# Optimization experiments

Hardware: AMD Instinct MI355X
Metric: run time of the kernel (lower is better)

The kernel has to match this reference:

```python
import jax, jax.numpy as jnp
import numpy as np

N_NODES = 100000
EPS = 1e-12


def gcn_conv(x, src, dst, ew, W, b, n):
    """PyG GCNConv with edge weights: add self-loops (w=1), symmetric norm,
    scatter-add messages from src to dst, then bias."""
    loop = jnp.arange(n)
    src2 = jnp.concatenate([src, loop])
    dst2 = jnp.concatenate([dst, loop])
    ew2 = jnp.concatenate([ew, jnp.ones((n,), dtype=ew.dtype)])
    deg = jax.ops.segment_sum(ew2, dst2, num_segments=n)
    dinv = jnp.where(deg > 0, jax.lax.rsqrt(jnp.where(deg > 0, deg, 1.0)), 0.0)
    norm = dinv[src2] * ew2 * dinv[dst2]  # [E+N]
    xw = x @ W.T                           # [N, H]
    msg = xw[src2] * norm[:, None]         # [E+N, H]  (memory-bound gather)
    out = jax.ops.segment_sum(msg, dst2, num_segments=n)
    return out + b


def setup_inputs() -> dict:
    key = jax.random.key(0)
    ks = jax.random.split(key, 12)
    N, E, D_IN, H, FE = N_NODES, 1600000, 256, 128, 8
    x = jax.random.normal(ks[0], (N, D_IN), dtype=jnp.float32)
    edge_index = jax.random.randint(ks[1], (2, E), 0, N, dtype=jnp.int64)
    edge_attr = jax.random.uniform(ks[2], (E, FE), dtype=jnp.float32)
    s_in = 1.0 / np.sqrt(D_IN)
    s_h = 1.0 / np.sqrt(H)
    W_in = jax.random.uniform(ks[3], (H, D_IN), minval=-s_in, maxval=s_in)
    b_in = jax.random.uniform(ks[4], (H,), minval=-s_in, maxval=s_in)
    W1 = jax.random.uniform(ks[5], (H, H), minval=-s_h, maxval=s_h)
    b1 = jax.random.uniform(ks[6], (H,), minval=-s_h, maxval=s_h)
    W2 = jax.random.uniform(ks[7], (H, H), minval=-s_h, maxval=s_h)
    b2 = jax.random.uniform(ks[8], (H,), minval=-s_h, maxval=s_h)
    W_out = jax.random.uniform(ks[9], (H, H), minval=-s_h, maxval=s_h)
    b_out = jax.random.uniform(ks[10], (H,), minval=-s_h, maxval=s_h)
    return {"x": x, "edge_index": edge_index, "edge_attr": edge_attr,
            "W_in": W_in, "b_in": b_in, "W1": W1, "b1": b1,
            "W2": W2, "b2": b2, "W_out": W_out, "b_out": b_out}


def reference(x, edge_index, edge_attr, W_in, b_in, W1, b1, W2, b2, W_out, b_out):
    n = x.shape[0]
    src, dst = edge_index[0], edge_index[1]
    # edge weights: sum over edge features, then L2-normalize over edges
    ew = edge_attr.sum(axis=1)
    ew = ew / jnp.maximum(jnp.linalg.norm(ew), EPS)
    h = jax.nn.relu(x @ W_in.T + b_in)      # dropout = identity (eval)
    h = jax.nn.relu(gcn_conv(h, src, dst, ew, W1, b1, n))
    h = gcn_conv(h, src, dst, ew, W2, b2, n)
    return h @ W_out.T + b_out
```

## Files before the change

### kernel.cpp

```cpp
#include <hip/hip_runtime.h>
#include <hip/hip_bf16.h>
#include <math.h>


#define CAP 64
#define BN 256
#define BCAP 5120
#define CHUNK 2048
#define SRC_MASK 0x1FFFFu
#define Q_SCALE 16777216.0f
#define Q_INV   5.9604644775390625e-8f
#define GSTRIDE 1024

typedef __attribute__((ext_vector_type(8))) short bf16x8;
typedef __attribute__((ext_vector_type(2))) float f32x2;
typedef __attribute__((ext_vector_type(4))) float f32x4;
typedef __attribute__((ext_vector_type(4))) unsigned int u32x4;

#if __has_builtin(__builtin_amdgcn_cvt_pk_f32_fp8)
#define DEC_SCALE 5.9604644775390625e-8f
__device__ __forceinline__ f32x2 dec2(unsigned short t) {
  return __builtin_amdgcn_cvt_pk_f32_fp8((int)(unsigned)t, false);
}
#else
#define DEC_SCALE 7.922816251426434e28f
__device__ __forceinline__ f32x2 dec2(unsigned short t) {
  f32x2 r;
  r.x = __builtin_bit_cast(float, (((unsigned)t & 0x80u) << 24) | (((unsigned)t & 0x7Fu) << 20));
  r.y = __builtin_bit_cast(float, (((unsigned)t & 0x8000u) << 16) | (((unsigned)t & 0x7F00u) << 12));
  return r;
}
#endif

__device__ __forceinline__ unsigned rne_bf16(float f) {
  const unsigned u = __builtin_bit_cast(unsigned, f);
  return (u + 0x7FFFu + ((u >> 16) & 1u)) >> 16;
}
__device__ __forceinline__ unsigned packsplit(float f) {
  const unsigned hb = rne_bf16(f);
  const float hf = __builtin_bit_cast(float, hb << 16);
  const unsigned lb = rne_bf16(f - hf);
  return (hb << 16) | (lb & 0xFFFFu);
}
__device__ __forceinline__ float unpk(unsigned p) {
  return __builtin_bit_cast(float, p & 0xFFFF0000u) +
         __builtin_bit_cast(float, p << 16);
}
__device__ __forceinline__ void split8(const f32x4 a, const f32x4 b,
                                       bf16x8& hi, bf16x8& lo) {
#pragma unroll
  for (int i = 0; i < 8; ++i) {
    const float f = (i < 4) ? a[i] : b[i - 4];
    const unsigned hb = rne_bf16(f);
    hi[i] = (short)hb;
    const float hf = __builtin_bit_cast(float, hb << 16);
    lo[i] = (short)rne_bf16(f - hf);
  }
}
__device__ __forceinline__ unsigned char enc_e4m3(float v) {
  const float a = v * 0x1p-120f;
  unsigned bits = __builtin_bit_cast(unsigned, a);
  const unsigned sgn = (bits >> 24) & 0x80u;
  bits &= 0x7FFFFFFFu;
  unsigned u7 = (bits + 0x7FFFFu + ((bits >> 20) & 1u)) >> 20;
  if (u7 > 0x7Eu) u7 = 0x7Eu;
  return (unsigned char)(sgn | u7);
}

__global__ void ew_wsplit_kernel(const float* __restrict__ ea, float* __restrict__ ew,
                                 float* __restrict__ partial, int E,
                                 const float* __restrict__ W_in, const float* __restrict__ W1,
                                 const float* __restrict__ W2, const float* __restrict__ W_out,
                                 short* __restrict__ whi, short* __restrict__ wlo) {
  __shared__ float red[256];
  const int tid = threadIdx.x;
  if (blockIdx.x < 1024) {
    float ss = 0.f;
    const int stride = 1024 * 256;
    for (int e = blockIdx.x * 256 + tid; e < E; e += stride) {
      const float4 a = *(const float4*)(ea + (size_t)e * 8);
      const float4 b = *(const float4*)(ea + (size_t)e * 8 + 4);
      const float s = ((a.x + a.y) + (a.z + a.w)) + ((b.x + b.y) + (b.z + b.w));
      ew[e] = s;
      ss = fmaf(s, s, ss);
    }
    red[tid] = ss;
    __syncthreads();
    for (int k = 128; k > 0; k >>= 1) {
      if (tid < k) red[tid] += red[tid + k];
      __syncthreads();
    }
    if (tid == 0) partial[blockIdx.x] = red[0];
  } else {
    const int i = (blockIdx.x - 1024) * 256 + tid;
    if (i < 81920) {
      float f;
      if (i < 32768) f = W_in[i];
      else if (i < 49152) f = W1[i - 32768];
      else if (i < 65536) f = W2[i - 49152];
      else f = W_out[i - 65536];
      const unsigned hb = rne_bf16(f);
      whi[i] = (short)hb;
      wlo[i] = (short)rne_bf16(f - __builtin_bit_cast(float, hb << 16));
    }
  }
}

__global__ void norm_cursor_kernel(const float* __restrict__ partial,
                                   float* __restrict__ invnorm,
                                   unsigned* __restrict__ cursors, int NB) {
  __shared__ float red[256];
  const int tid = threadIdx.x;
  if (blockIdx.x == 0) {
    float s = partial[tid] + partial[tid + 256] + partial[tid + 512] + partial[tid + 768];
    red[tid] = s;
    __syncthreads();
    for (int k = 128; k > 0; k >>= 1) {
      if (tid < k) red[tid] += red[tid + k];
      __syncthreads();
    }
    if (tid == 0) invnorm[0] = 1.0f / fmaxf(sqrtf(red[0]), 1e-12f);
  } else {
    const int i = (blockIdx.x - 1) * 256 + tid;
    if (i < NB) cursors[i * 16] = (unsigned)i * BCAP;
  }
}

__global__ __launch_bounds__(512, 4) void bin_gemmin_kernel(
    const int* __restrict__ src, const int* __restrict__ dst,
    const float* __restrict__ ew, const float* __restrict__ invnorm,
    unsigned* __restrict__ cursors, unsigned long long* __restrict__ buckets,
    int E, int NB, int nbin,
    const float* __restrict__ X, const short* __restrict__ Whi,
    const short* __restrict__ Wlo, const float* __restrict__ bias,
    unsigned* __restrict__ Ypk, int ntiles) {
  __shared__ __align__(16) char smem[36864];
  const int tid = threadIdx.x;
  if ((int)blockIdx.x < nbin) {
    unsigned long long* recs = (unsigned long long*)smem;
    unsigned* hist = (unsigned*)(smem + 32768);
    unsigned* base = (unsigned*)(smem + 34816);
    const int e0 = blockIdx.x * CHUNK;
    const int n = min(CHUNK, E - e0);
    for (int i = tid; i < NB; i += 512) hist[i] = 0;
    __syncthreads();
    const float inv = invnorm[0];
    for (int i = tid; i < n; i += 512) {
      const int s = src[e0 + i];
      const int d = dst[e0 + i];
      const float w = ew[e0 + i] * inv;
      const unsigned q = (unsigned)fminf(fmaf(w, Q_SCALE, 0.5f), 32767.0f);
      recs[i] = ((unsigned long long)(((unsigned)d << 15) | q) << 32) | (unsigned)s;
      atomicAdd(&hist[d >> 8], 1u);
    }
    __syncthreads();
    for (int i = tid; i < NB; i += 512) {
      const unsigned c = hist[i];
      base[i] = c ? atomicAdd(&cursors[i * 16], c) : 0u;
      hist[i] = 0;
    }
    __syncthreads();
    for (int i = tid; i < n; i += 512) {
      const unsigned long long r = recs[i];
      const unsigned b = ((unsigned)(r >> 32) >> 15) >> 8;
      const unsigned pos = base[b] + atomicAdd(&hist[b], 1u);
      if (pos < (b + 1) * BCAP) buckets[pos] = r;
    }
  } else {
    constexpr int K = 256, KT = 8, RT = 2, CPR = 32;
    short* hi_p = (short*)smem;
    short* lo_p = (short*)(smem + 16384);
    const int lane = tid & 63, wave = tid >> 6;
    const int lrow = lane & 15, loct = lane >> 4;

    bf16x8 bhi[KT], blo[KT];
    const int col = wave * 16 + lrow;
#pragma unroll
    for (int kt = 0; kt < KT; ++kt) {
      const int off = col * K + kt * 32 + loct * 8;
      bhi[kt] = *(const bf16x8*)&Whi[off];
      blo[kt] = *(const bf16x8*)&Wlo[off];
    }
    const float bv = bias[col];

    const int r0c = tid >> 5, r1c = (tid + 512) >> 5;
    const int cc = tid & 31;
    f32x4 sa[2][2];
    const int vb = (int)blockIdx.x - nbin;

    int t = vb;
    {
      const int tl = (t < ntiles) ? t : 0;
      const float* xp0 = X + ((size_t)tl * 32 + r0c) * K + cc * 8;
      const float* xp1 = X + ((size_t)tl * 32 + r1c) * K + cc * 8;
      sa[0][0] = *(const f32x4*)xp0; sa[0][1] = *(const f32x4*)(xp0 + 4);
      sa[1][0] = *(const f32x4*)xp1; sa[1][1] = *(const f32x4*)(xp1 + 4);
    }
    while (t < ntiles) {
      {
        const int slot0 = r0c * CPR + (cc ^ (r0c & 7));
        const int slot1 = r1c * CPR + (cc ^ (r1c & 7));
        bf16x8 h, l;
        split8(sa[0][0], sa[0][1], h, l);
        *(bf16x8*)&hi_p[slot0 * 8] = h;
        *(bf16x8*)&lo_p[slot0 * 8] = l;
        split8(sa[1][0], sa[1][1], h, l);
        *(bf16x8*)&hi_p[slot1 * 8] = h;
        *(bf16x8*)&lo_p[slot1 * 8] = l;
      }
      __syncthreads();
      const int tn = t + GSTRIDE;
      {
        const int tl = (tn < ntiles) ? tn : 0;
        const float* xp0 = X + ((size_t)tl * 32 + r0c) * K + cc * 8;
        const float* xp1 = X + ((size_t)tl * 32 + r1c) * K + cc * 8;
        sa[0][0] = *(const f32x4*)xp0; sa[0][1] = *(const f32x4*)(xp0 + 4);
        sa[1][0] = *(const f32x4*)xp1; sa[1][1] = *(const f32x4*)(xp1 + 4);
      }
      f32x4 acc[RT];
#pragma unroll
      for (int rt = 0; rt < RT; ++rt) acc[rt] = f32x4{0.f, 0.f, 0.f, 0.f};
#pragma unroll
      for (int kt = 0; kt < KT; ++kt) {
        bf16x8 ahi[RT], alo[RT];
#pragma unroll
        for (int rt = 0; rt < RT; ++rt) {
          const int lr = rt * 16 + lrow;
          const int off = (lr * CPR + ((kt * 4 + loct) ^ (lr & 7))) * 8;
          ahi[rt] = *(const bf16x8*)&hi_p[off];
          alo[rt] = *(const bf16x8*)&lo_p[off];
        }
#pragma unroll
        for (int rt = 0; rt < RT; ++rt) {
          acc[rt] = __builtin_amdgcn_mfma_f32_16x16x32_bf16(ahi[rt], bhi[kt], acc[rt], 0, 0, 0);
          acc[rt] = __builtin_amdgcn_mfma_f32_16x16x32_bf16(ahi[rt], blo[kt], acc[rt], 0, 0, 0);
          acc[rt] = __builtin_amdgcn_mfma_f32_16x16x32_bf16(alo[rt], bhi[kt], acc[rt], 0, 0, 0);
        }
      }
      const int rbase = t * 32;
#pragma unroll
      for (int rt = 0; rt < RT; ++rt)
#pragma unroll
        for (int r = 0; r < 4; ++r) {
          const float v = fmaxf(acc[rt][r] + bv, 0.f);
          Ypk[(size_t)(rbase + rt * 16 + loct * 4 + r) * 128 + col] = packsplit(v);
        }
      t = tn;
      __syncthreads();
    }
  }
}

__global__ __launch_bounds__(256) void build_kernel(
    const unsigned long long* __restrict__ buckets,
    const unsigned* __restrict__ cursors,
    unsigned* __restrict__ cv, float* __restrict__ dinv,
    int* __restrict__ fillg, int N) {
  __shared__ unsigned cvl[BN * CAP];
  __shared__ unsigned fl[BN];
  const int tid = threadIdx.x;
  const int b = blockIdx.x;
  const int n0 = b << 8;
  for (int i = tid; i < BN * CAP; i += 256) cvl[i] = 0;
  for (int i = tid; i < BN; i += 256) fl[i] = 0;
  __syncthreads();
  const unsigned start = (unsigned)b * BCAP;
  const int cnt = min((int)(cursors[b * 16] - start), BCAP);
  for (int i = tid; i < cnt; i += 256) {
    const unsigned long long r = buckets[start + i];
    const unsigned hi = (unsigned)(r >> 32);
    const unsigned dlo = (hi >> 15) & (BN - 1);
    const unsigned q = hi & 0x7FFFu;
    const unsigned p = atomicAdd(&fl[dlo], 1u);
    if (p < CAP) cvl[(dlo << 6) + p] = (q << 17) | (unsigned)(r & 0xFFFFFFFFu);
  }
  __syncthreads();
  if (n0 + tid < N) {
    const int c = min((int)fl[tid], CAP);
    unsigned qs = 0;
    for (int i = 0; i < c; ++i) qs += cvl[(tid << 6) + i] >> 17;
    dinv[n0 + tid] = rsqrtf(fmaf((float)qs, Q_INV, 1.0f));
    fillg[n0 + tid] = c;
  }
  const u32x4* s = (const u32x4*)cvl;
  u32x4* g = (u32x4*)(cv + ((size_t)b << 14));
  for (int i = tid; i < BN * CAP / 4; i += 256)
    __builtin_nontemporal_store(s[i], &g[i]);
}

template <bool OUT_FP8, bool OUT_F32, bool HAS_BIAS, bool RELU>
__device__ __forceinline__ void gemm_pk_body(
    char* smem, int vb, int stride,
    const unsigned* __restrict__ Xpk, const short* __restrict__ Whi,
    const short* __restrict__ Wlo, const float* __restrict__ bias,
    unsigned* __restrict__ Ypk, unsigned char* __restrict__ Yf8,
    float* __restrict__ Yf32, int ntiles) {
  constexpr int K = 128, KT = 4, CT = 2, RT = 2, CPR = 16;
  short* hi_p = (short*)smem;
  short* lo_p = (short*)(smem + 8192);
  const int tid = threadIdx.x;
  const int lane = tid & 63, wave = tid >> 6;
  const int lrow = lane & 15, loct = lane >> 4;

  bf16x8 bhi[CT][KT], blo[CT][KT];
#pragma unroll
  for (int ct = 0; ct < CT; ++ct) {
    const int col = (wave * CT + ct) * 16 + lrow;
#pragma unroll
    for (int kt = 0; kt < KT; ++kt) {
      const int off = col * K + kt * 32 + loct * 8;
      bhi[ct][kt] = *(const bf16x8*)&Whi[off];
      blo[ct][kt] = *(const bf16x8*)&Wlo[off];
    }
  }
  float bv[CT];
  if constexpr (HAS_BIAS) {
#pragma unroll
    for (int ct = 0; ct < CT; ++ct) bv[ct] = bias[(wave * CT + ct) * 16 + lrow];
  }

  const int r0c = tid >> 4, r1c = (tid + 256) >> 4;
  const int cc = tid & 15;
  u32x4 sa[2][2];

  int t = vb;
  {
    const int tl = (t < ntiles) ? t : 0;
    const unsigned* xp0 = Xpk + ((size_t)tl * 32 + r0c) * K + cc * 8;
    const unsigned* xp1 = Xpk + ((size_t)tl * 32 + r1c) * K + cc * 8;
    sa[0][0] = *(const u32x4*)xp0; sa[0][1] = *(const u32x4*)(xp0 + 4);
    sa[1][0] = *(const u32x4*)xp1; sa[1][1] = *(const u32x4*)(xp1 + 4);
  }
  while (t < ntiles) {
#pragma unroll
    for (int p = 0; p < 2; ++p) {
      const int r = p ? r1c : r0c;
      const int slot = r * CPR + (cc ^ (r & 7));
      const u32x4 a = sa[p][0], b = sa[p][1];
      u32x4 wh, wl;
      wh[0] = (a[1] & 0xFFFF0000u) | (a[0] >> 16);
      wh[1] = (a[3] & 0xFFFF0000u) | (a[2] >> 16);
      wh[2] = (b[1] & 0xFFFF0000u) | (b[0] >> 16);
      wh[3] = (b[3] & 0xFFFF0000u) | (b[2] >> 16);
      wl[0] = (a[1] << 16) | (a[0] & 0xFFFFu);
      wl[1] = (a[3] << 16) | (a[2] & 0xFFFFu);
      wl[2] = (b[1] << 16) | (b[0] & 0xFFFFu);
      wl[3] = (b[3] << 16) | (b[2] & 0xFFFFu);
      *(u32x4*)&hi_p[slot * 8] = wh;
      *(u32x4*)&lo_p[slot * 8] = wl;
    }
    __syncthreads();
    const int tn = t + stride;
    {
      const int tl = (tn < ntiles) ? tn : 0;
      const unsigned* xp0 = Xpk + ((size_t)tl * 32 + r0c) * K + cc * 8;
      const unsigned* xp1 = Xpk + ((size_t)tl * 32 + r1c) * K + cc * 8;
      sa[0][0] = *(const u32x4*)xp0; sa[0][1] = *(const u32x4*)(xp0 + 4);
      sa[1][0] = *(const u32x4*)xp1; sa[1][1] = *(const u32x4*)(xp1 + 4);
    }
    f32x4 acc[RT][CT];
#pragma unroll
    for (int rt = 0; rt < RT; ++rt)
#pragma unroll
      for (int ct = 0; ct < CT; ++ct) acc[rt][ct] = f32x4{0.f, 0.f, 0.f, 0.f};
#pragma unroll
    for (int kt = 0; kt < KT; ++kt) {
      bf16x8 ahi[RT], alo[RT];
#pragma unroll
      for (int rt = 0; rt < RT; ++rt) {
        const int lr = rt * 16 + lrow;
        const int off = (lr * CPR + ((kt * 4 + loct) ^ (lr & 7))) * 8;
        ahi[rt] = *(const bf16x8*)&hi_p[off];
        alo[rt] = *(const bf16x8*)&lo_p[off];
      }
#pragma unroll
      for (int rt = 0; rt < RT; ++rt)
#pragma unroll
        for (int ct = 0; ct < CT; ++ct) {
          acc[rt][ct] = __builtin_amdgcn_mfma_f32_16x16x32_bf16(ahi[rt], bhi[ct][kt], acc[rt][ct], 0, 0, 0);
          acc[rt][ct] = __builtin_amdgcn_mfma_f32_16x16x32_bf16(ahi[rt], blo[ct][kt], acc[rt][ct], 0, 0, 0);
          acc[rt][ct] = __builtin_amdgcn_mfma_f32_16x16x32_bf16(alo[rt], bhi[ct][kt], acc[rt][ct], 0, 0, 0);
        }
    }
    const int rbase = t * 32;
#pragma unroll
    for (int rt = 0; rt < RT; ++rt)
#pragma unroll
      for (int ct = 0; ct < CT; ++ct) {
        const int col = (wave * CT + ct) * 16 + lrow;
#pragma unroll
        for (int r = 0; r < 4; ++r) {
          float v = acc[rt][ct][r];
          if constexpr (HAS_BIAS) v += bv[ct];
          if constexpr (RELU) v = fmaxf(v, 0.f);
          const size_t idx = (size_t)(rbase + rt * 16 + loct * 4 + r) * 128 + col;
          if constexpr (OUT_F32) {
            Yf32[idx] = v;
          } else {
            Ypk[idx] = packsplit(v);
            if constexpr (OUT_FP8) Yf8[idx] = enc_e4m3(v);
          }
        }
      }
    t = tn;
    __syncthreads();
  }
}

__global__ __launch_bounds__(256, 4) void valfin_gemmpk_kernel(
    unsigned* __restrict__ cv, const int* __restrict__ fillg,
    const float* __restrict__ dinv, int N,
    const unsigned* __restrict__ Xpk, const short* __restrict__ Whi,
    const short* __restrict__ Wlo, unsigned* __restrict__ Ypk,
    unsigned char* __restrict__ Yf8, int ntiles) {
  __shared__ __align__(16) char smem[16384];
  if (blockIdx.x < 512) {
    const int total = N * (CAP / 4);
    for (int i = blockIdx.x * 256 + threadIdx.x; i < total; i += 512 * 256) {
      const int n = i >> 4;
      const int slot0 = (i & 15) * 4;
      const int c = fillg[n];
      if (slot0 >= c) continue;
      const float dn = dinv[n];
      u32x4 q = *(u32x4*)&cv[((size_t)n << 6) + slot0];
#pragma unroll
      for (int j = 0; j < 4; ++j) {
        if (slot0 + j < c) {
          const unsigned s = q[j] & SRC_MASK;
          const float wv = dinv[s] * dn * ((float)(q[j] >> 17) * Q_INV);
          const unsigned w15 = (unsigned)fminf(fmaf(wv, Q_SCALE, 0.5f), 32767.0f);
          q[j] = (w15 << 17) | s;
        }
      }
      *(u32x4*)&cv[((size_t)n << 6) + slot0] = q;
    }
  } else {
    gemm_pk_body<true, false, false, false>(smem, (int)blockIdx.x - 512, GSTRIDE,
                                            Xpk, Whi, Wlo, nullptr, Ypk, Yf8,
                                            nullptr, ntiles);
  }
}

template <bool OUT_FP8, bool OUT_F32, bool HAS_BIAS, bool RELU>
__global__ __launch_bounds__(256, 4) void gemm_pk_pipe(
    const unsigned* __restrict__ Xpk, const short* __restrict__ Whi,
    const short* __restrict__ Wlo, const float* __restrict__ bias,
    unsigned* __restrict__ Ypk, unsigned char* __restrict__ Yf8,
    float* __restrict__ Yf32, int ntiles) {
  __shared__ __align__(16) char smem[16384];
  gemm_pk_body<OUT_FP8, OUT_F32, HAS_BIAS, RELU>(smem, (int)blockIdx.x, GSTRIDE,
                                                 Xpk, Whi, Wlo, bias, Ypk, Yf8,
                                                 Yf32, ntiles);
}

template <bool RELU>
__global__ __launch_bounds__(256) void gather_kernel(const unsigned* __restrict__ xw,
                                                     const unsigned char* __restrict__ xf8,
                                                     const int* __restrict__ fill,
                                                     const unsigned* __restrict__ cv,
                                                     const float* __restrict__ dinv,
                                                     const float* __restrict__ bias,
                                                     unsigned* __restrict__ out, int N) {
  const int lane = threadIdx.x & 63;
  const int n = (blockIdx.x * blockDim.x + threadIdx.x) >> 6;
  if (n >= N) return;
  const int f = lane * 2;
  const float dn = dinv[n];
  const float dn2 = dn * dn;
  const uint2 xs = *(const uint2*)&xw[(size_t)n * 128 + f];
  float ax = dn2 * unpk(xs.x);
  float ay = dn2 * unpk(xs.y);
  const unsigned* row = cv + ((size_t)n << 6);
  const int c = min(fill[n], CAP);
  for (int e = 0; e < c; e += 16) {
    u32x4 cg[4];
    cg[0] = *(const u32x4*)&row[e];
    cg[1] = *(const u32x4*)&row[e + 4];
    cg[2] = *(const u32x4*)&row[e + 8];
    cg[3] = *(const u32x4*)&row[e + 12];
    unsigned cr[16];
#pragma unroll
    for (int g = 0; g < 4; ++g) {
      cr[g * 4 + 0] = cg[g][0]; cr[g * 4 + 1] = cg[g][1];
      cr[g * 4 + 2] = cg[g][2]; cr[g * 4 + 3] = cg[g][3];
    }
    unsigned short t[16];
#pragma unroll
    for (int j = 0; j < 16; ++j)
      t[j] = *(const unsigned short*)&xf8[(size_t)(cr[j] & SRC_MASK) * 128 + f];
#pragma unroll
    for (int j = 0; j < 16; ++j) {
      const float vs = (float)(cr[j] >> 17) * DEC_SCALE;
      const f32x2 xy = dec2(t[j]);
      ax = fmaf(vs, xy.x, ax);
      ay = fmaf(vs, xy.y, ay);
    }
  }
  const float2 bb = *(const float2*)&bias[f];
  float o0 = ax + bb.x, o1 = ay + bb.y;
  if (RELU) { o0 = fmaxf(o0, 0.f); o1 = fmaxf(o1, 0.f); }
  uint2 res;
  res.x = packsplit(o0);
  res.y = packsplit(o1);
  *(uint2*)&out[(size_t)n * 128 + f] = res;
}

extern "C" void kernel_launch(void* const* d_in, const int* in_sizes, int n_in,
                              void* d_out, int out_size, void* d_ws, size_t ws_size,
                              hipStream_t stream) {
  const float* x     = (const float*)d_in[0];
  const int*   eidx  = (const int*)d_in[1];
  const float* ea    = (const float*)d_in[2];
  const float* W_in  = (const float*)d_in[3];
  const float* b_in  = (const float*)d_in[4];
  const float* W1    = (const float*)d_in[5];
  const float* b1    = (const float*)d_in[6];
  const float* W2    = (const float*)d_in[7];
  const float* b2    = (const float*)d_in[8];
  const float* W_out = (const float*)d_in[9];
  const float* b_out = (const float*)d_in[10];

  const int E = in_sizes[2] / 8;
  const int N = in_sizes[0] / 256;
  const int* srcp = eidx;
  const int* dstp = eidx + E;
  const int NB = (N + BN - 1) / BN;
  const int nbin = (E + CHUNK - 1) / CHUNK;

  char* w = (char*)d_ws;
  size_t o = 0;
  auto take = [&](size_t bytes) -> void* {
    void* p = w + o;
    o += (bytes + 255) & ~(size_t)255;
    return p;
  };
  float* ew            = (float*)take((size_t)E * 4);
  float* partial       = (float*)take(1024 * 4);
  float* invnorm       = (float*)take(256);
  float* dinv          = (float*)take((size_t)N * 4);
  int*   fillg         = (int*)take((size_t)N * 4);
  short* whi           = (short*)take(81920 * 2);
  short* wlo           = (short*)take(81920 * 2);
  unsigned* cursors    = (unsigned*)take((size_t)NB * 16 * 4);
  unsigned long long* buckets = (unsigned long long*)take((size_t)NB * BCAP * 8);
  unsigned* cv         = (unsigned*)take((size_t)NB * BN * CAP * 4);
  unsigned* buf0       = (unsigned*)take((size_t)N * 128 * 4);
  unsigned* buf1       = (unsigned*)take((size_t)N * 128 * 4);
  unsigned char* buff8 = (unsigned char*)take((size_t)N * 128);
  float* outp          = (float*)d_out;

  const int ntiles = N / 32;

  ew_wsplit_kernel<<<1344, 256, 0, stream>>>(ea, ew, partial, E,
                                             W_in, W1, W2, W_out, whi, wlo);
  norm_cursor_kernel<<<1 + (NB + 255) / 256, 256, 0, stream>>>(partial, invnorm, cursors, NB);
  bin_gemmin_kernel<<<nbin + GSTRIDE, 512, 0, stream>>>(
      srcp, dstp, ew, invnorm, cursors, buckets, E, NB, nbin,
      x, whi, wlo, b_in, buf0, ntiles);
  build_kernel<<<NB, 256, 0, stream>>>(buckets, cursors, cv, dinv, fillg, N);
  valfin_gemmpk_kernel<<<512 + GSTRIDE, 256, 0, stream>>>(
      cv, fillg, dinv, N, buf0, whi + 32768, wlo + 32768, buf1, buff8, ntiles);
  gather_kernel<true><<<(N * 64 + 255) / 256, 256, 0, stream>>>(buf1, buff8, fillg, cv, dinv, b1, buf0, N);
  gemm_pk_pipe<true, false, false, false><<<GSTRIDE, 256, 0, stream>>>(
      buf0, whi + 49152, wlo + 49152, nullptr, buf1, buff8, nullptr, ntiles);
  gather_kernel<false><<<(N * 64 + 255) / 256, 256, 0, stream>>>(buf1, buff8, fillg, cv, dinv, b2, buf0, N);
  gemm_pk_pipe<false, true, true, false><<<GSTRIDE, 256, 0, stream>>>(
      buf0, whi + 65536, wlo + 65536, b_out, nullptr, nullptr, outp, ntiles);
}
```

Before: 289.1 us.

## Locally sort edge records by bucket in LDS before coalesced scatter

Doubles the edge chunk per binning block and adds an in-block counting sort. A wave-level prefix scan over the per-bucket histogram produces local offsets, records are permuted in shared memory, and then contiguous runs go out to each global bucket. The aim is to turn random 8-byte global scatter writes into mostly contiguous ones and to halve the number of global cursor atomics per edge. In exchange it uses more LDS, adds barriers, and assumes NB fits in 512 threads (NBMAX 400), which could lower occupancy for the GEMM blocks that share this kernel.

```diff
diff --git a/kernel.cpp b/kernel.cpp
--- a/kernel.cpp
+++ b/kernel.cpp
@@ -6,7 +6,8 @@
 #define CAP 64
 #define BN 256
 #define BCAP 5120
-#define CHUNK 2048
+#define CHUNK 4096
+#define NBMAX 400
 #define SRC_MASK 0x1FFFFu
 #define Q_SCALE 16777216.0f
 #define Q_INV   5.9604644775390625e-8f
@@ -134,15 +135,18 @@
     const float* __restrict__ X, const short* __restrict__ Whi,
     const short* __restrict__ Wlo, const float* __restrict__ bias,
     unsigned* __restrict__ Ypk, int ntiles) {
-  __shared__ __align__(16) char smem[36864];
+  __shared__ __align__(16) char smem[53952];
+  __shared__ unsigned wsb[8];
   const int tid = threadIdx.x;
   if ((int)blockIdx.x < nbin) {
     unsigned long long* recs = (unsigned long long*)smem;
-    unsigned* hist = (unsigned*)(smem + 32768);
-    unsigned* base = (unsigned*)(smem + 34816);
+    unsigned* perm = (unsigned*)(smem + 32768);
+    unsigned* hist = (unsigned*)(smem + 49152);
+    unsigned* base = (unsigned*)(smem + 50752);
+    unsigned* lofs = (unsigned*)(smem + 52352);
     const int e0 = blockIdx.x * CHUNK;
     const int n = min(CHUNK, E - e0);
-    for (int i = tid; i < NB; i += 512) hist[i] = 0;
+    for (int i = tid; i < NBMAX; i += 512) hist[i] = 0;
     __syncthreads();
     const float inv = invnorm[0];
     for (int i = tid; i < n; i += 512) {
@@ -154,17 +158,39 @@
       atomicAdd(&hist[d >> 8], 1u);
     }
     __syncthreads();
-    for (int i = tid; i < NB; i += 512) {
-      const unsigned c = hist[i];
-      base[i] = c ? atomicAdd(&cursors[i * 16], c) : 0u;
-      hist[i] = 0;
+    {
+      const unsigned x = (tid < NB) ? hist[tid] : 0u;
+      unsigned xi = x;
+#pragma unroll
+      for (int d = 1; d < 64; d <<= 1) {
+        const unsigned y = __shfl_up(xi, d, 64);
+        if ((tid & 63) >= d) xi += y;
+      }
+      if ((tid & 63) == 63) wsb[tid >> 6] = xi;
+      __syncthreads();
+      if (tid == 0) {
+        unsigned s = 0;
+        for (int w2 = 0; w2 < 8; ++w2) { const unsigned t = wsb[w2]; wsb[w2] = s; s += t; }
+      }
+      __syncthreads();
+      if (tid < NB) {
+        lofs[tid] = wsb[tid >> 6] + xi - x;
+        base[tid] = x ? atomicAdd(&cursors[tid * 16], x) : 0u;
+        hist[tid] = 0;
+      }
     }
     __syncthreads();
     for (int i = tid; i < n; i += 512) {
-      const unsigned long long r = recs[i];
-      const unsigned b = ((unsigned)(r >> 32) >> 15) >> 8;
-      const unsigned pos = base[b] + atomicAdd(&hist[b], 1u);
-      if (pos < (b + 1) * BCAP) buckets[pos] = r;
+      const unsigned b = (unsigned)(recs[i] >> 55);
+      const unsigned rank = atomicAdd(&hist[b], 1u);
+      perm[lofs[b] + rank] = (b << 12) | (unsigned)i;
+    }
+    __syncthreads();
+    for (int p = tid; p < n; p += 512) {
+      const unsigned u = perm[p];
+      const unsigned b = u >> 12;
+      const unsigned g = base[b] + ((unsigned)p - lofs[b]);
+      if (g < (b + 1) * BCAP) buckets[g] = recs[u & 4095u];
     }
   } else {
     constexpr int K = 256, KT = 8, RT = 2, CPR = 32;
```

Result: faster. 277.2 us (-4.1%).
